# Kernel tuning notes

Measured on AMD Instinct MI355X. Metric: run time of the kernel, lower is better.

## Reference

```python
import jax, jax.numpy as jnp
import numpy as np

B, T, D, H = 2, 2048, 1024, 16
DK = D // H

def setup_inputs() -> dict:
    key = jax.random.key(0)
    ks = jax.random.split(key, 12)
    s = 1.0 / np.sqrt(D)
    inp = {
        'Q': jax.random.normal(ks[0], (B, T, D), jnp.float32),
        'K': jax.random.normal(ks[1], (B, T, D), jnp.float32),
        'V': jax.random.normal(ks[2], (B, T, D), jnp.float32),
        'mask': jnp.tril(jnp.ones((T, T), jnp.int32))[None, None],  # causal [1,1,T,T]
        'Wq_w': jax.random.normal(ks[3], (D, D), jnp.float32) * s,
        'Wq_b': jax.random.normal(ks[4], (D,), jnp.float32) * s,
        'Wk_w': jax.random.normal(ks[5], (D, D), jnp.float32) * s,
        'Wk_b': jax.random.normal(ks[6], (D,), jnp.float32) * s,
        'Wv_w': jax.random.normal(ks[7], (D, D), jnp.float32) * s,
        'Wv_b': jax.random.normal(ks[8], (D,), jnp.float32) * s,
        'Wo_w': jax.random.normal(ks[9], (D, D), jnp.float32) * s,
        'Wo_b': jax.random.normal(ks[10], (D,), jnp.float32) * s,
    }
    return inp

def reference(Q, K, V, mask, Wq_w, Wq_b, Wk_w, Wk_b, Wv_w, Wv_b, Wo_w, Wo_b):
    b, tq, c = Q.shape
    tk = K.shape[1]
    q = (Q @ Wq_w + Wq_b).reshape(b, tq, H, DK).transpose(0, 2, 1, 3)  # [B,H,Tq,dk]
    k = (K @ Wk_w + Wk_b).reshape(b, tk, H, DK).transpose(0, 2, 1, 3)
    v = (V @ Wv_w + Wv_b).reshape(b, tk, H, DK).transpose(0, 2, 1, 3)
    scores = jnp.einsum('bhqd,bhkd->bhqk', q, k) / jnp.sqrt(jnp.float32(DK))
    scores = jnp.where(mask == 0, jnp.float32(-1e9), scores)
    attn = jax.nn.softmax(scores, axis=-1)
    out = jnp.einsum('bhqk,bhkd->bhqd', attn, v)
    out = out.transpose(0, 2, 1, 3).reshape(b, tq, c)
    return out @ Wo_w + Wo_b
```

## Files before the change

kernel.cpp:

```cpp
#include <hip/hip_runtime.h>
#include <hip/hip_bf16.h>

#define NB 2
#define NT 2048
#define ND 1024
#define NH 16
#define NDK 64

typedef __attribute__((ext_vector_type(8))) short bf16x8;
typedef __attribute__((ext_vector_type(4))) float f32x4;

static __device__ __forceinline__ short f2bf(float f) {
  union { float f; unsigned u; } c; c.f = f;
  unsigned u = c.u;
  u += 0x7FFF + ((u >> 16) & 1);
  return (short)(u >> 16);
}

static __device__ __forceinline__ unsigned cvt_pk_bf16(float lo, float hi) {
  unsigned r;
  asm("v_cvt_pk_bf16_f32 %0, %1, %2" : "=v"(r) : "v"(lo), "v"(hi));
  return r;
}

static __device__ __forceinline__ void gload16(const void* g, void* l) {
  __builtin_amdgcn_global_load_lds((const __attribute__((address_space(1))) void*)g,
                                   (__attribute__((address_space(3))) void*)l, 16, 0, 0);
}

__global__ void prep_kernel(const float* __restrict__ Q, const float* __restrict__ Ki,
                            const float* __restrict__ V,
                            short* __restrict__ Qb, short* __restrict__ Kb, short* __restrict__ Vb,
                            const float* __restrict__ W0, const float* __restrict__ W1,
                            const float* __restrict__ W2, const float* __restrict__ W3,
                            short* __restrict__ T0, short* __restrict__ T1,
                            short* __restrict__ T2, short* __restrict__ T3) {
  __shared__ float t[32][33];
  int d = blockIdx.x, tid = threadIdx.x;
  if (d < 6144) {
    int z = d >> 11;
    int i = (d & 2047) * 256 + tid;
    const float* src = z == 0 ? Q : (z == 1 ? Ki : V);
    short* dst       = z == 0 ? Qb : (z == 1 ? Kb : Vb);
    const float4* s4 = (const float4*)src + (size_t)i * 2;
    float4 a = s4[0], b = s4[1];
    bf16x8 o;
    o[0] = f2bf(a.x); o[1] = f2bf(a.y); o[2] = f2bf(a.z); o[3] = f2bf(a.w);
    o[4] = f2bf(b.x); o[5] = f2bf(b.y); o[6] = f2bf(b.z); o[7] = f2bf(b.w);
    *((bf16x8*)dst + i) = o;
  } else {
    int dd = d - 6144;
    int z = dd >> 10;
    int rem = dd & 1023;
    const float* W = z == 0 ? W0 : (z == 1 ? W1 : (z == 2 ? W2 : W3));
    short* Wt      = z == 0 ? T0 : (z == 1 ? T1 : (z == 2 ? T2 : T3));
    int n0 = (rem & 31) * 32, k0 = (rem >> 5) * 32;
    int tx = tid & 31, ty = tid >> 5;
    for (int i = ty; i < 32; i += 8) t[i][tx] = W[(size_t)(k0 + i) * ND + n0 + tx];
    __syncthreads();
    for (int i = ty; i < 32; i += 8) Wt[(size_t)(n0 + i) * ND + k0 + tx] = f2bf(t[tx][i]);
  }
}

template <int MODE, int BN>
__global__ __launch_bounds__(256, 3) void gemm_bt(
    const short* __restrict__ A0, const short* __restrict__ A1, const short* __restrict__ A2,
    const short* __restrict__ W0, const short* __restrict__ W1, const short* __restrict__ W2,
    const float* __restrict__ b0, const float* __restrict__ b1, const float* __restrict__ b2,
    void* o0, void* o1, void* o2)
{
  constexpr int K = ND;
  constexpr int NI = BN / 32;
  constexpr int NNB = ND / BN;
  constexpr int NZ = (MODE == 0) ? 3 : 1;
  constexpr int NWPX = NZ * 32 * NNB / 8;
  __shared__ short As[2][128 * 32];
  __shared__ short Bs[2][BN * 32];

  int d = blockIdx.x;
  int work = (d & 7) * NWPX + (d >> 3);
  int z = work / (32 * NNB);
  int rem = work % (32 * NNB);
  int m0 = (rem / NNB) * 128, n0 = (rem % NNB) * BN;

  const short* A    = z == 0 ? A0 : (z == 1 ? A1 : A2);
  const short* Wt   = z == 0 ? W0 : (z == 1 ? W1 : W2);
  const float* bias = z == 0 ? b0 : (z == 1 ? b1 : b2);
  void* out         = z == 0 ? o0 : (z == 1 ? o1 : o2);
  float scl = (MODE == 0 && z == 0) ? 0.18033688011112042f : 1.0f;

  int tid = threadIdx.x, wid = tid >> 6, lane = tid & 63;
  int wr = wid >> 1, wc = wid & 1;
  int r16 = lane & 15, l4 = lane >> 4;

  auto stage = [&](int buf, int kt) {
    int row = (lane >> 2);
    int c8 = (lane & 3) * 8;
    {
      int rbase = wid * 32;
      const short* ga = A + (size_t)(m0 + rbase + row) * K + kt * 32 + c8;
      gload16(ga,          &As[buf][rbase * 32]);
      gload16(ga + 16 * K, &As[buf][(rbase + 16) * 32]);
    }
    if constexpr (BN == 128) {
      int rbase = wid * 32;
      const short* gb = Wt + (size_t)(n0 + rbase + row) * K + kt * 32 + c8;
      gload16(gb,          &Bs[buf][rbase * 32]);
      gload16(gb + 16 * K, &Bs[buf][(rbase + 16) * 32]);
    } else {
      int rbase = wid * 16;
      const short* gb = Wt + (size_t)(n0 + rbase + row) * K + kt * 32 + c8;
      gload16(gb,          &Bs[buf][rbase * 32]);
    }
  };

  f32x4 acc[4][NI] = {};
  stage(0, 0);
  __syncthreads();

  for (int kt = 0; kt < K / 32; ++kt) {
    int cur = kt & 1;
    if (kt + 1 < K / 32) stage(cur ^ 1, kt + 1);
    bf16x8 af[4], bfv[NI];
    int kk = l4 * 8;
#pragma unroll
    for (int mi = 0; mi < 4; mi++)
      af[mi] = *(const bf16x8*)&As[cur][(wr * 64 + mi * 16 + r16) * 32 + kk];
#pragma unroll
    for (int ni = 0; ni < NI; ni++)
      bfv[ni] = *(const bf16x8*)&Bs[cur][(wc * (BN / 2) + ni * 16 + r16) * 32 + kk];
#pragma unroll
    for (int mi = 0; mi < 4; mi++)
#pragma unroll
      for (int ni = 0; ni < NI; ni++)
        acc[mi][ni] = __builtin_amdgcn_mfma_f32_16x16x32_bf16(af[mi], bfv[ni], acc[mi][ni], 0, 0, 0);
    __syncthreads();
  }

  int mb = m0 + wr * 64, nb = n0 + wc * (BN / 2);
#pragma unroll
  for (int mi = 0; mi < 4; mi++)
#pragma unroll
    for (int ni = 0; ni < NI; ni++) {
      int n = nb + ni * 16 + r16;
      float bv = bias[n];
      if constexpr (MODE == 0) {
        int h = n >> 6, dk = n & 63;
        if (z == 2) {
          int m0_ = mb + mi * 16 + l4 * 4;
          int bI = m0_ >> 11, t0 = m0_ & (NT - 1);
          int bh = bI * NH + h;
          short4 s4;
          s4.x = f2bf(acc[mi][ni][0] + bv);
          s4.y = f2bf(acc[mi][ni][1] + bv);
          s4.z = f2bf(acc[mi][ni][2] + bv);
          s4.w = f2bf(acc[mi][ni][3] + bv);
          *(short4*)&((short*)out)[(size_t)bh * 131072 + (dk >> 4) * 32768 +
                                   (t0 >> 3) * 128 + (dk & 15) * 8 + (t0 & 7)] = s4;
        } else if (z == 1) {
#pragma unroll
          for (int r = 0; r < 4; r++) {
            int m = mb + mi * 16 + l4 * 4 + r;
            int bI = m >> 11, t = m & (NT - 1);
            int bh = bI * NH + h;
            ((short*)out)[(size_t)bh * 131072 + (t >> 4) * 1024 + (dk >> 3) * 128 +
                          (t & 15) * 8 + (dk & 7)] = f2bf(acc[mi][ni][r] + bv);
          }
        } else {
#pragma unroll
          for (int r = 0; r < 4; r++) {
            int m = mb + mi * 16 + l4 * 4 + r;
            int bI = m >> 11, t = m & (NT - 1);
            ((short*)out)[((((size_t)bI * NH + h) * NT + t) << 6) + dk] = f2bf((acc[mi][ni][r] + bv) * scl);
          }
        }
      } else {
#pragma unroll
        for (int r = 0; r < 4; r++) {
          int m = mb + mi * 16 + l4 * 4 + r;
          ((float*)out)[(size_t)m * ND + n] = acc[mi][ni][r] + bv;
        }
      }
    }
}

__global__ __launch_bounds__(256) void attn_kernel(
    const short* __restrict__ q, const short* __restrict__ k, const short* __restrict__ vt,
    short* __restrict__ O)
{
  struct SH {
    union {
      short p2[4][2][16][72];
      struct {
        f32x4 obuf[4][2][2][64];
        float ol[4][32];
      } mg;
    };
  };
  __shared__ SH sh;

  int d = blockIdx.x;
  int xcd = d & 7, jj = d >> 3;
  int bh = xcd * 4 + (jj >> 6);
  int qg = 63 - (jj & 63);
  int b = bh >> 4, h = bh & 15;
  int tid = threadIdx.x, wid = tid >> 6, lane = tid & 63;
  int r16 = lane & 15, l4 = lane >> 4;
  size_t hb = (size_t)bh * NT * NDK;
  const short* qh = q + hb;
  const short* kh = k + hb;
  const short* vh = vt + hb;
  int qw = qg * 32;

  bf16x8 qa[2][2];
#pragma unroll
  for (int rf = 0; rf < 2; rf++)
#pragma unroll
    for (int kf = 0; kf < 2; kf++)
      qa[rf][kf] = *(const bf16x8*)(qh + (size_t)(qw + rf * 16 + r16) * NDK + kf * 32 + l4 * 8);

  f32x4 of[2][4] = {};
  float l0 = 0.f, l1 = 0.f;

  int nt = (qw + 95) >> 6;

  bf16x8 kfr[4][2];
  if (wid < nt) {
#pragma unroll
    for (int cf = 0; cf < 4; cf++) {
      const short* kb_ = kh + (size_t)((wid * 64 >> 4) + cf) * 1024 + lane * 8;
      kfr[cf][0] = *(const bf16x8*)kb_;
      kfr[cf][1] = *(const bf16x8*)(kb_ + 512);
    }
  }

  for (int kt = wid; kt < nt; kt += 4) {
    int kv0 = kt * 64;
    f32x4 sf[2][4] = {};

#pragma unroll
    for (int cf = 0; cf < 4; cf++) {
      sf[0][cf] = __builtin_amdgcn_mfma_f32_16x16x32_bf16(kfr[cf][0], qa[0][0], sf[0][cf], 0, 0, 0);
      sf[0][cf] = __builtin_amdgcn_mfma_f32_16x16x32_bf16(kfr[cf][1], qa[0][1], sf[0][cf], 0, 0, 0);
    }
#pragma unroll
    for (int cf = 0; cf < 4; cf++) {
      sf[1][cf] = __builtin_amdgcn_mfma_f32_16x16x32_bf16(kfr[cf][0], qa[1][0], sf[1][cf], 0, 0, 0);
      sf[1][cf] = __builtin_amdgcn_mfma_f32_16x16x32_bf16(kfr[cf][1], qa[1][1], sf[1][cf], 0, 0, 0);
    }

    {
      int ktn = (kt + 4 < nt) ? kt + 4 : kt;
      int kvn = ktn * 64;
#pragma unroll
      for (int cf = 0; cf < 4; cf++) {
        const short* kb_ = kh + (size_t)((kvn >> 4) + cf) * 1024 + lane * 8;
        kfr[cf][0] = *(const bf16x8*)kb_;
        kfr[cf][1] = *(const bf16x8*)(kb_ + 512);
      }
    }

    bf16x8 vb[4][2];
#pragma unroll
    for (int df = 0; df < 4; df++)
#pragma unroll
      for (int kf = 0; kf < 2; kf++)
        vb[df][kf] = *(const bf16x8*)(vh + df * 32768 + (kv0 >> 3) * 128 + kf * 512 + lane * 8);

    bool nm = (kv0 + 63 > qw);

    if (nm) {
#pragma unroll
      for (int cf = 0; cf < 4; cf++)
#pragma unroll
        for (int r = 0; r < 4; r++) {
          int kvi = kv0 + cf * 16 + l4 * 4 + r;
          if (kvi > qw + r16) sf[0][cf][r] = -1e30f;
        }
    }
    {
      float rs = 0.f;
#pragma unroll
      for (int cf = 0; cf < 4; cf++) {
        float p0 = __builtin_amdgcn_exp2f(sf[0][cf][0]);
        float p1 = __builtin_amdgcn_exp2f(sf[0][cf][1]);
        float p2v = __builtin_amdgcn_exp2f(sf[0][cf][2]);
        float p3 = __builtin_amdgcn_exp2f(sf[0][cf][3]);
        rs += (p0 + p1) + (p2v + p3);
        unsigned w0 = cvt_pk_bf16(p0, p1);
        unsigned w1 = cvt_pk_bf16(p2v, p3);
        *(int2*)&sh.p2[wid][0][r16][cf * 16 + l4 * 4] = make_int2((int)w0, (int)w1);
      }
      l0 += rs;
    }
#pragma unroll
    for (int kf = 0; kf < 2; kf++) {
      bf16x8 pa = *(const bf16x8*)&sh.p2[wid][0][r16][kf * 32 + l4 * 8];
#pragma unroll
      for (int df = 0; df < 4; df++)
        of[0][df] = __builtin_amdgcn_mfma_f32_16x16x32_bf16(vb[df][kf], pa, of[0][df], 0, 0, 0);
    }

    if (nm) {
#pragma unroll
      for (int cf = 0; cf < 4; cf++)
#pragma unroll
        for (int r = 0; r < 4; r++) {
          int kvi = kv0 + cf * 16 + l4 * 4 + r;
          if (kvi > qw + 16 + r16) sf[1][cf][r] = -1e30f;
        }
    }
    {
      float rs = 0.f;
#pragma unroll
      for (int cf = 0; cf < 4; cf++) {
        float p0 = __builtin_amdgcn_exp2f(sf[1][cf][0]);
        float p1 = __builtin_amdgcn_exp2f(sf[1][cf][1]);
        float p2v = __builtin_amdgcn_exp2f(sf[1][cf][2]);
        float p3 = __builtin_amdgcn_exp2f(sf[1][cf][3]);
        rs += (p0 + p1) + (p2v + p3);
        unsigned w0 = cvt_pk_bf16(p0, p1);
        unsigned w1 = cvt_pk_bf16(p2v, p3);
        *(int2*)&sh.p2[wid][1][r16][cf * 16 + l4 * 4] = make_int2((int)w0, (int)w1);
      }
      l1 += rs;
    }
#pragma unroll
    for (int kf = 0; kf < 2; kf++) {
      bf16x8 pa = *(const bf16x8*)&sh.p2[wid][1][r16][kf * 32 + l4 * 8];
#pragma unroll
      for (int df = 0; df < 4; df++)
        of[1][df] = __builtin_amdgcn_mfma_f32_16x16x32_bf16(vb[df][kf], pa, of[1][df], 0, 0, 0);
    }
  }

  l0 += __shfl_xor(l0, 16); l0 += __shfl_xor(l0, 32);
  l1 += __shfl_xor(l1, 16); l1 += __shfl_xor(l1, 32);

  __syncthreads();
  if (l4 == 0) {
    sh.mg.ol[wid][r16] = l0;
    sh.mg.ol[wid][16 + r16] = l1;
  }
#pragma unroll
  for (int pass = 0; pass < 2; ++pass) {
#pragma unroll
    for (int rf = 0; rf < 2; rf++)
#pragma unroll
      for (int dfp = 0; dfp < 2; dfp++)
        sh.mg.obuf[wid][rf][dfp][lane] = of[rf][2 * pass + dfp];
    __syncthreads();
    {
      int mrf = wid >> 1, mdfp = wid & 1, mdf = 2 * pass + mdfp;
      int row = mrf * 16 + r16;
      float lst = sh.mg.ol[0][row] + sh.mg.ol[1][row] + sh.mg.ol[2][row] + sh.mg.ol[3][row];
      float rinv = 1.0f / lst;
      f32x4 o0 = sh.mg.obuf[0][mrf][mdfp][lane];
      f32x4 o1 = sh.mg.obuf[1][mrf][mdfp][lane];
      f32x4 o2 = sh.mg.obuf[2][mrf][mdfp][lane];
      f32x4 o3 = sh.mg.obuf[3][mrf][mdfp][lane];
      float v0 = (o0[0] + o1[0] + o2[0] + o3[0]) * rinv;
      float v1 = (o0[1] + o1[1] + o2[1] + o3[1]) * rinv;
      float v2 = (o0[2] + o1[2] + o2[2] + o3[2]) * rinv;
      float v3 = (o0[3] + o1[3] + o2[3] + o3[3]) * rinv;
      int t = qw + mrf * 16 + r16;
      *(int2*)&O[(size_t)(b * NT + t) * ND + h * 64 + mdf * 16 + l4 * 4] =
          make_int2((int)cvt_pk_bf16(v0, v1), (int)cvt_pk_bf16(v2, v3));
    }
    __syncthreads();
  }
}

extern "C" void kernel_launch(void* const* d_in, const int* in_sizes, int n_in,
                              void* d_out, int out_size, void* d_ws, size_t ws_size,
                              hipStream_t stream)
{
  const float* Q  = (const float*)d_in[0];
  const float* Ki = (const float*)d_in[1];
  const float* V  = (const float*)d_in[2];
  const float* Wq = (const float*)d_in[4];  const float* bq = (const float*)d_in[5];
  const float* Wk = (const float*)d_in[6];  const float* bk = (const float*)d_in[7];
  const float* Wv = (const float*)d_in[8];  const float* bv = (const float*)d_in[9];
  const float* Wo = (const float*)d_in[10]; const float* bo = (const float*)d_in[11];

  short* ws = (short*)d_ws;
  const size_t M4 = (size_t)4 * 1024 * 1024;
  short* Qb  = ws;
  short* Kb  = ws + M4;
  short* Vb  = ws + 2 * M4;
  short* qp  = ws + 3 * M4;
  short* kp  = ws + 4 * M4;
  short* vtp = ws + 5 * M4;
  short* Wqt = ws + 6 * M4;
  short* Wkt = Wqt + 1024 * 1024;
  short* Wvt = Wkt + 1024 * 1024;
  short* Wot = Wvt + 1024 * 1024;
  short* Obuf = Qb;

  prep_kernel<<<10240, 256, 0, stream>>>(Q, Ki, V, Qb, Kb, Vb,
                                         Wq, Wk, Wv, Wo, Wqt, Wkt, Wvt, Wot);

  gemm_bt<0, 128><<<768, 256, 0, stream>>>(Qb, Kb, Vb, Wqt, Wkt, Wvt,
                                           bq, bk, bv, qp, kp, vtp);
  attn_kernel<<<2048, 256, 0, stream>>>(qp, kp, vtp, Obuf);
  gemm_bt<1, 64><<<512, 256, 0, stream>>>(Obuf, Obuf, Obuf, Wot, Wot, Wot,
                                          bo, bo, bo, d_out, d_out, d_out);
}
```

Before: 115.1 us.

## Restructure attention: per-wave query rows with shared double-buffered K/V tiles in LDS

Before, each 256-thread block handled 32 query rows and split the KV range across 4 waves, then merged partial outputs through shared memory. Now each block handles 128 query rows with one 32-row slice per wave. All waves share K/V tiles staged into double-buffered LDS through async global-to-LDS loads, and the launch drops from 2048 to 512 blocks. This removes the cross-wave output merge and makes K/V global traffic 4x more reusable. In exchange there are per-tile __syncthreads barriers, fewer blocks for load balance, and causal imbalance, since waves whose rows are past the diagonal idle at barriers.

```diff
diff --git a/kernel.cpp b/kernel.cpp
--- a/kernel.cpp
+++ b/kernel.cpp
@@ -188,21 +188,16 @@
     const short* __restrict__ q, const short* __restrict__ k, const short* __restrict__ vt,
     short* __restrict__ O)
 {
-  struct SH {
-    union {
-      short p2[4][2][16][72];
-      struct {
-        f32x4 obuf[4][2][2][64];
-        float ol[4][32];
-      } mg;
-    };
-  };
-  __shared__ SH sh;
+  __shared__ short kv[2][8192];
+  __shared__ short p2[4][2][16][72];
 
   int d = blockIdx.x;
-  int xcd = d & 7, jj = d >> 3;
-  int bh = xcd * 4 + (jj >> 6);
-  int qg = 63 - (jj & 63);
+  int halfsel = d >> 8;
+  int dd = d & 255;
+  int xcd = dd & 7, jj = dd >> 3;
+  int bh = xcd * 4 + (jj & 3);
+  int qbi = jj >> 2;
+  int qb = halfsel == 0 ? (15 - qbi) : qbi;
   int b = bh >> 4, h = bh & 15;
   int tid = threadIdx.x, wid = tid >> 6, lane = tid & 63;
   int r16 = lane & 15, l4 = lane >> 4;
@@ -210,7 +205,10 @@
   const short* qh = q + hb;
   const short* kh = k + hb;
   const short* vh = vt + hb;
-  int qw = qg * 32;
+
+  int qw = qb * 128 + wid * 32;
+  int nt = 2 * qb + 2;
+  int sb = wid * 512 + lane * 8;
 
   bf16x8 qa[2][2];
 #pragma unroll
@@ -222,50 +220,36 @@
   f32x4 of[2][4] = {};
   float l0 = 0.f, l1 = 0.f;
 
-  int nt = (qw + 95) >> 6;
-
-  bf16x8 kfr[4][2];
-  if (wid < nt) {
+  auto stage = [&](int nbuf, int kv0s) {
+    const short* kb = kh + (size_t)(kv0s >> 4) * 1024;
+    gload16(kb + sb,        &kv[nbuf][sb]);
+    gload16(kb + 2048 + sb, &kv[nbuf][2048 + sb]);
+    int o1 = sb, o2 = 2048 + sb;
+    gload16(vh + (size_t)(o1 >> 10) * 32768 + (kv0s >> 3) * 128 + (o1 & 1023),
+            &kv[nbuf][4096 + o1]);
+    gload16(vh + (size_t)(o2 >> 10) * 32768 + (kv0s >> 3) * 128 + (o2 & 1023),
+            &kv[nbuf][4096 + o2]);
+  };
+
+  stage(0, 0);
+
+  for (int kt = 0; kt < nt; ++kt) {
+    int buf = kt & 1;
+    int kv0 = kt * 64;
+    __syncthreads();
+    if (kt + 1 < nt) stage(buf ^ 1, kv0 + 64);
+    if (kv0 > qw + 31) continue;
+
+    f32x4 sf[2][4] = {};
 #pragma unroll
     for (int cf = 0; cf < 4; cf++) {
-      const short* kb_ = kh + (size_t)((wid * 64 >> 4) + cf) * 1024 + lane * 8;
-      kfr[cf][0] = *(const bf16x8*)kb_;
-      kfr[cf][1] = *(const bf16x8*)(kb_ + 512);
-    }
-  }
-
-  for (int kt = wid; kt < nt; kt += 4) {
-    int kv0 = kt * 64;
-    f32x4 sf[2][4] = {};
-
-#pragma unroll
-    for (int cf = 0; cf < 4; cf++) {
-      sf[0][cf] = __builtin_amdgcn_mfma_f32_16x16x32_bf16(kfr[cf][0], qa[0][0], sf[0][cf], 0, 0, 0);
-      sf[0][cf] = __builtin_amdgcn_mfma_f32_16x16x32_bf16(kfr[cf][1], qa[0][1], sf[0][cf], 0, 0, 0);
-    }
-#pragma unroll
-    for (int cf = 0; cf < 4; cf++) {
-      sf[1][cf] = __builtin_amdgcn_mfma_f32_16x16x32_bf16(kfr[cf][0], qa[1][0], sf[1][cf], 0, 0, 0);
-      sf[1][cf] = __builtin_amdgcn_mfma_f32_16x16x32_bf16(kfr[cf][1], qa[1][1], sf[1][cf], 0, 0, 0);
-    }
-
-    {
-      int ktn = (kt + 4 < nt) ? kt + 4 : kt;
-      int kvn = ktn * 64;
-#pragma unroll
-      for (int cf = 0; cf < 4; cf++) {
-        const short* kb_ = kh + (size_t)((kvn >> 4) + cf) * 1024 + lane * 8;
-        kfr[cf][0] = *(const bf16x8*)kb_;
-        kfr[cf][1] = *(const bf16x8*)(kb_ + 512);
-      }
-    }
-
-    bf16x8 vb[4][2];
-#pragma unroll
-    for (int df = 0; df < 4; df++)
-#pragma unroll
-      for (int kf = 0; kf < 2; kf++)
-        vb[df][kf] = *(const bf16x8*)(vh + df * 32768 + (kv0 >> 3) * 128 + kf * 512 + lane * 8);
+      bf16x8 k0 = *(const bf16x8*)&kv[buf][cf * 1024 + lane * 8];
+      bf16x8 k1 = *(const bf16x8*)&kv[buf][cf * 1024 + 512 + lane * 8];
+      sf[0][cf] = __builtin_amdgcn_mfma_f32_16x16x32_bf16(k0, qa[0][0], sf[0][cf], 0, 0, 0);
+      sf[0][cf] = __builtin_amdgcn_mfma_f32_16x16x32_bf16(k1, qa[0][1], sf[0][cf], 0, 0, 0);
+      sf[1][cf] = __builtin_amdgcn_mfma_f32_16x16x32_bf16(k0, qa[1][0], sf[1][cf], 0, 0, 0);
+      sf[1][cf] = __builtin_amdgcn_mfma_f32_16x16x32_bf16(k1, qa[1][1], sf[1][cf], 0, 0, 0);
+    }
 
     bool nm = (kv0 + 63 > qw);
 
@@ -289,16 +273,18 @@
         rs += (p0 + p1) + (p2v + p3);
         unsigned w0 = cvt_pk_bf16(p0, p1);
         unsigned w1 = cvt_pk_bf16(p2v, p3);
-        *(int2*)&sh.p2[wid][0][r16][cf * 16 + l4 * 4] = make_int2((int)w0, (int)w1);
+        *(int2*)&p2[wid][0][r16][cf * 16 + l4 * 4] = make_int2((int)w0, (int)w1);
       }
       l0 += rs;
     }
 #pragma unroll
     for (int kf = 0; kf < 2; kf++) {
-      bf16x8 pa = *(const bf16x8*)&sh.p2[wid][0][r16][kf * 32 + l4 * 8];
-#pragma unroll
-      for (int df = 0; df < 4; df++)
-        of[0][df] = __builtin_amdgcn_mfma_f32_16x16x32_bf16(vb[df][kf], pa, of[0][df], 0, 0, 0);
+      bf16x8 pa = *(const bf16x8*)&p2[wid][0][r16][kf * 32 + l4 * 8];
+#pragma unroll
+      for (int df = 0; df < 4; df++) {
+        bf16x8 vf = *(const bf16x8*)&kv[buf][4096 + df * 1024 + kf * 512 + lane * 8];
+        of[0][df] = __builtin_amdgcn_mfma_f32_16x16x32_bf16(vf, pa, of[0][df], 0, 0, 0);
+      }
     }
 
     if (nm) {
@@ -321,53 +307,34 @@
         rs += (p0 + p1) + (p2v + p3);
         unsigned w0 = cvt_pk_bf16(p0, p1);
         unsigned w1 = cvt_pk_bf16(p2v, p3);
-        *(int2*)&sh.p2[wid][1][r16][cf * 16 + l4 * 4] = make_int2((int)w0, (int)w1);
+        *(int2*)&p2[wid][1][r16][cf * 16 + l4 * 4] = make_int2((int)w0, (int)w1);
       }
       l1 += rs;
     }
 #pragma unroll
     for (int kf = 0; kf < 2; kf++) {
-      bf16x8 pa = *(const bf16x8*)&sh.p2[wid][1][r16][kf * 32 + l4 * 8];
-#pragma unroll
-      for (int df = 0; df < 4; df++)
-        of[1][df] = __builtin_amdgcn_mfma_f32_16x16x32_bf16(vb[df][kf], pa, of[1][df], 0, 0, 0);
+      bf16x8 pa = *(const bf16x8*)&p2[wid][1][r16][kf * 32 + l4 * 8];
+#pragma unroll
+      for (int df = 0; df < 4; df++) {
+        bf16x8 vf = *(const bf16x8*)&kv[buf][4096 + df * 1024 + kf * 512 + lane * 8];
+        of[1][df] = __builtin_amdgcn_mfma_f32_16x16x32_bf16(vf, pa, of[1][df], 0, 0, 0);
+      }
     }
   }
 
   l0 += __shfl_xor(l0, 16); l0 += __shfl_xor(l0, 32);
   l1 += __shfl_xor(l1, 16); l1 += __shfl_xor(l1, 32);
-
-  __syncthreads();
-  if (l4 == 0) {
-    sh.mg.ol[wid][r16] = l0;
-    sh.mg.ol[wid][16 + r16] = l1;
-  }
-#pragma unroll
-  for (int pass = 0; pass < 2; ++pass) {
-#pragma unroll
-    for (int rf = 0; rf < 2; rf++)
-#pragma unroll
-      for (int dfp = 0; dfp < 2; dfp++)
-        sh.mg.obuf[wid][rf][dfp][lane] = of[rf][2 * pass + dfp];
-    __syncthreads();
-    {
-      int mrf = wid >> 1, mdfp = wid & 1, mdf = 2 * pass + mdfp;
-      int row = mrf * 16 + r16;
-      float lst = sh.mg.ol[0][row] + sh.mg.ol[1][row] + sh.mg.ol[2][row] + sh.mg.ol[3][row];
-      float rinv = 1.0f / lst;
-      f32x4 o0 = sh.mg.obuf[0][mrf][mdfp][lane];
-      f32x4 o1 = sh.mg.obuf[1][mrf][mdfp][lane];
-      f32x4 o2 = sh.mg.obuf[2][mrf][mdfp][lane];
-      f32x4 o3 = sh.mg.obuf[3][mrf][mdfp][lane];
-      float v0 = (o0[0] + o1[0] + o2[0] + o3[0]) * rinv;
-      float v1 = (o0[1] + o1[1] + o2[1] + o3[1]) * rinv;
-      float v2 = (o0[2] + o1[2] + o2[2] + o3[2]) * rinv;
-      float v3 = (o0[3] + o1[3] + o2[3] + o3[3]) * rinv;
-      int t = qw + mrf * 16 + r16;
-      *(int2*)&O[(size_t)(b * NT + t) * ND + h * 64 + mdf * 16 + l4 * 4] =
-          make_int2((int)cvt_pk_bf16(v0, v1), (int)cvt_pk_bf16(v2, v3));
-    }
-    __syncthreads();
+#pragma unroll
+  for (int rf = 0; rf < 2; rf++) {
+    float rinv = 1.0f / (rf == 0 ? l0 : l1);
+    int t = qw + rf * 16 + r16;
+#pragma unroll
+    for (int df = 0; df < 4; df++) {
+      unsigned w0 = cvt_pk_bf16(of[rf][df][0] * rinv, of[rf][df][1] * rinv);
+      unsigned w1 = cvt_pk_bf16(of[rf][df][2] * rinv, of[rf][df][3] * rinv);
+      *(int2*)&O[(size_t)(b * NT + t) * ND + h * 64 + df * 16 + l4 * 4] =
+          make_int2((int)w0, (int)w1);
+    }
   }
 }
 
@@ -402,7 +369,7 @@
 
   gemm_bt<0, 128><<<768, 256, 0, stream>>>(Qb, Kb, Vb, Wqt, Wkt, Wvt,
                                            bq, bk, bv, qp, kp, vtp);
-  attn_kernel<<<2048, 256, 0, stream>>>(qp, kp, vtp, Obuf);
+  attn_kernel<<<512, 256, 0, stream>>>(qp, kp, vtp, Obuf);
   gemm_bt<1, 64><<<512, 256, 0, stream>>>(Obuf, Obuf, Obuf, Wot, Wot, Wot,
                                           bo, bo, bo, d_out, d_out, d_out);
 }
```

New measurement: 118.6 us. 1.03x slower.
